# Performance work log

Measured on AMD Instinct MI355X. Metric: run time of the kernel, lower is better.

The kernel has to match this reference:

```python
import jax, jax.numpy as jnp
import numpy as np

BZ, T, D, DFF, E, BEAMS = 128, 32, 768, 3072, 8, 2


def setup_inputs() -> dict:
    key = jax.random.key(0)
    ks = jax.random.split(key, 4)
    s = 0.02
    return {
        "x": jax.random.normal(ks[0], (BZ, T, D), jnp.float32),
        "attention_mask": jnp.ones((BZ, T), jnp.float32),
        "Wg": jax.random.normal(ks[1], (D, E), jnp.float32) * s,   # gate Linear(D,E,bias=False)
        "W1": jax.random.normal(ks[2], (E, D, DFF), jnp.float32) * s,
        "b1": jnp.zeros((E, DFF), jnp.float32),
        "W2": jax.random.normal(ks[3], (E, DFF, D), jnp.float32) * s,
        "b2": jnp.zeros((E, D), jnp.float32),
    }


def reference(x, attention_mask, Wg, W1, b1, W2, b2):
    # forward_gate: module builds its own all-ones mask regardless of input mask
    mask = jnp.ones((x.shape[0], x.shape[1]), x.dtype)
    x_avg = (x * mask[..., None]).sum(1) / mask[..., None].sum(1)   # [bz, D]
    prob = jax.nn.softmax(x_avg @ Wg, axis=-1)                       # [bz, E]
    # beam_search (layer_judge='first', pre-route): topk on exp(log(softmax)) == softmax probs
    scores = jnp.exp(jnp.log(prob))
    topv, topi = jax.lax.top_k(scores, BEAMS)                        # [bz, beams]
    beam_scores = topv.reshape(-1)                                   # [bz*beams]
    expert_route = topi.reshape(-1, 1)                                # [bz*beams, 1]
    sel = expert_route[:, -1]
    # replicate x per beam: [bz*beams, T, D]
    x_rep = jnp.broadcast_to(x[:, None], (x.shape[0], BEAMS, x.shape[1], x.shape[2]))
    x_rep = x_rep.reshape(-1, x.shape[1], x.shape[2])
    # per-sample expert FFN dispatch (dense masked loop over the E=8 experts)
    out = jnp.zeros_like(x_rep)
    for e in range(E):
        h = jax.nn.gelu(jnp.einsum('nsd,df->nsf', x_rep, W1[e]) + b1[e], approximate=False)
        ye = jnp.einsum('nsf,fd->nsd', h, W2[e]) + b2[e]
        out = jnp.where((sel == e)[:, None, None], ye, out)
    return (out, beam_scores, expert_route)
```

## Files before the change

kernel.cpp:

```cpp
#include <hip/hip_runtime.h>
#include <cstddef>
#include <cstdint>

#define BZd   128
#define Td    32
#define Dd    768
#define DFFd  3072
#define Ed    8
#define NBEAM 256
#define ROWS_TOT 8192
#define OUT_ELEMS 6291456
#define MAXTILES 72

typedef unsigned short u16;
typedef __attribute__((ext_vector_type(4))) unsigned short ushort4v;
typedef __attribute__((ext_vector_type(8))) short frag_ab;
typedef __attribute__((ext_vector_type(4))) float floatx4;

__device__ __forceinline__ u16 f2bf(float f) {
  unsigned int u = __builtin_bit_cast(unsigned int, f);
  u += 0x7FFFu + ((u >> 16) & 1u);
  return (u16)(u >> 16);
}

__device__ __forceinline__ void async_copy16(u16* lds, const u16* g) {
  __builtin_amdgcn_global_load_lds(
      (const __attribute__((address_space(1))) void*)g,
      (__attribute__((address_space(3))) void*)lds, 16, 0, 0);
}

__device__ __forceinline__ float gelu_fast(float x) {
  float z = 1.5957691216f * (x + 0.044715f * x * x * x);
  return x / (1.0f + __expf(-z));
}

__global__ __launch_bounds__(256) void route_convert_kernel(
    const float* __restrict__ x, const float* __restrict__ Wg,
    float* __restrict__ out, int* __restrict__ sel, u16* __restrict__ xbf) {
  int b = blockIdx.x;
  int t = threadIdx.x;
  __shared__ float red[256][8];
  float la[8];
#pragma unroll
  for (int e = 0; e < 8; e++) la[e] = 0.f;
  for (int d = t; d < Dd; d += 256) {
    const float* xp = x + (size_t)b * Td * Dd + d;
    float xa = 0.f;
#pragma unroll
    for (int tt = 0; tt < Td; tt++) xa += xp[(size_t)tt * Dd];
    xa *= (1.0f / 32.0f);
#pragma unroll
    for (int e = 0; e < 8; e++) la[e] += xa * Wg[d * 8 + e];
  }
#pragma unroll
  for (int e = 0; e < 8; e++) red[t][e] = la[e];
  __syncthreads();
  for (int s = 128; s > 0; s >>= 1) {
    if (t < s) {
#pragma unroll
      for (int e = 0; e < 8; e++) red[t][e] += red[t + s][e];
    }
    __syncthreads();
  }
  if (t == 0) {
    float lg[8];
#pragma unroll
    for (int e = 0; e < 8; e++) lg[e] = red[0][e];
    float mx = lg[0];
#pragma unroll
    for (int e = 1; e < 8; e++) mx = fmaxf(mx, lg[e]);
    float p[8];
    float sum = 0.f;
#pragma unroll
    for (int e = 0; e < 8; e++) { p[e] = __expf(lg[e] - mx); sum += p[e]; }
    float inv = 1.0f / sum;
#pragma unroll
    for (int e = 0; e < 8; e++) p[e] *= inv;
    int i0 = 0; float v0 = p[0];
#pragma unroll
    for (int e = 1; e < 8; e++) if (p[e] > v0) { v0 = p[e]; i0 = e; }
    int i1 = -1; float v1 = -1.0f;
#pragma unroll
    for (int e = 0; e < 8; e++) if (e != i0 && p[e] > v1) { v1 = p[e]; i1 = e; }
    float* bs = out + OUT_ELEMS;
    float* er = out + OUT_ELEMS + NBEAM;
    bs[2 * b] = v0; bs[2 * b + 1] = v1;
    er[2 * b] = (float)i0; er[2 * b + 1] = (float)i1;
    sel[2 * b] = i0; sel[2 * b + 1] = i1;
  }
  const float* xp = x + (size_t)b * Td * Dd;
  u16* op = xbf + (size_t)b * Td * Dd;
#pragma unroll
  for (int k = 0; k < 24; k++) {
    int flat = (k * 256 + t) * 4;
    float4 v = *(const float4*)(xp + flat);
    ushort4v pv = {f2bf(v.x), f2bf(v.y), f2bf(v.z), f2bf(v.w)};
    *(ushort4v*)(op + flat) = pv;
  }
}

__global__ __launch_bounds__(256) void bucket_kernel(
    const int* __restrict__ sel, int* __restrict__ perm, int4* __restrict__ tiles) {
  __shared__ int ssel[NBEAM];
  __shared__ int scnt[8];
  __shared__ int soff[8];
  __shared__ int sperm[NBEAM];
  int t = threadIdx.x;
  ssel[t] = sel[t];
  __syncthreads();
  if (t == 0) {
    for (int e = 0; e < 8; e++) scnt[e] = 0;
    for (int n = 0; n < NBEAM; n++) scnt[ssel[n]]++;
    int o = 0;
    for (int e = 0; e < 8; e++) { soff[e] = o; o += scnt[e]; }
  }
  __syncthreads();
  if (t < 8) {
    int idx = soff[t];
    for (int n = 0; n < NBEAM; n++)
      if (ssel[n] == t) sperm[idx++] = n;
  }
  if (t == 0) {
    int tt = 0;
    for (int e = 0; e < 8; e++) {
      int nr = scnt[e] * 32;
      int base = soff[e] * 32;
      for (int r0 = 0; r0 < nr; r0 += 128) {
        tiles[tt] = make_int4(e, base + r0, min(128, nr - r0), 0);
        tt++;
      }
    }
    for (; tt < MAXTILES; tt++) tiles[tt] = make_int4(-1, 0, 0, 0);
  }
  __syncthreads();
  perm[t] = sperm[t];
}

__global__ __launch_bounds__(256) void transpose_all_kernel(
    const float* __restrict__ W1, u16* __restrict__ w1t,
    const float* __restrict__ W2, u16* __restrict__ w2t, int f0, int FC) {
  __shared__ u16 tile[64][65];
  int z = blockIdx.z, bx = blockIdx.x, by = blockIdx.y;
  int t = threadIdx.x;
  const float* ip; u16* op; int ld_in, ld_out;
  if (z < 8) {
    int e = z;
    ld_in = DFFd; ld_out = Dd;
    ip = W1 + (size_t)e * Dd * DFFd + (size_t)(bx * 64) * DFFd + (f0 + by * 64);
    op = w1t + (size_t)e * FC * Dd + (size_t)(by * 64) * Dd + bx * 64;
  } else {
    int e = z - 8;
    ld_in = Dd; ld_out = FC;
    ip = W2 + (size_t)e * DFFd * Dd + (size_t)(f0 + by * 64) * Dd + bx * 64;
    op = w2t + (size_t)e * Dd * FC + (size_t)(bx * 64) * FC + by * 64;
  }
  int rr = t >> 4, cc4 = (t & 15) * 4;
#pragma unroll
  for (int i = 0; i < 4; i++) {
    int r = rr + 16 * i;
    float4 v = *(const float4*)(ip + (size_t)r * ld_in + cc4);
    tile[r][cc4 + 0] = f2bf(v.x);
    tile[r][cc4 + 1] = f2bf(v.y);
    tile[r][cc4 + 2] = f2bf(v.z);
    tile[r][cc4 + 3] = f2bf(v.w);
  }
  __syncthreads();
  int ccw = t >> 4, r4 = (t & 15) * 4;
#pragma unroll
  for (int i = 0; i < 4; i++) {
    int cc = ccw + 16 * i;
    ushort4v pv = {tile[r4 + 0][cc], tile[r4 + 1][cc], tile[r4 + 2][cc], tile[r4 + 3][cc]};
    *(ushort4v*)(op + (size_t)cc * ld_out + r4) = pv;
  }
}

__global__ __launch_bounds__(256) void gemm1_kernel(
    const u16* __restrict__ xbf, const u16* __restrict__ w1t,
    const float* __restrict__ b1, const int* __restrict__ perm,
    const int4* __restrict__ tiles, u16* __restrict__ h, int f0, int FC) {
  int4 meta = tiles[blockIdx.y];
  int e = meta.x;
  if (e < 0) return;
  int grow0 = meta.y, nrows = meta.z;
  int bx = blockIdx.x;

  __shared__ __align__(16) u16 As[2][128 * 32];
  __shared__ __align__(16) u16 Bs[2][128 * 32];

  int t = threadIdx.x;
  int l = t & 63, w = t >> 6;
  int wm = w & 1, wn = w >> 1;
  int lrow = l & 15, lquad = l >> 4;

  const u16* ag[2]; const u16* bg[2];
  int lbase[2];
#pragma unroll
  for (int j = 0; j < 2; j++) {
    int s = j * 256 + t;
    int m = s >> 2;
    int koff = ((s & 3) ^ ((m >> 1) & 3)) * 8;
    int bidx = (grow0 >> 5) + (m >> 5);
    bidx = bidx < NBEAM ? bidx : NBEAM - 1;
    int batch = perm[bidx] >> 1;
    ag[j] = xbf + ((size_t)batch * Td + (m & 31)) * Dd + koff;
    bg[j] = w1t + ((size_t)e * FC + bx * 128 + m) * Dd + koff;
    lbase[j] = (j * 256 + w * 64) * 8;
  }

  int aoff[4], boff[4];
#pragma unroll
  for (int i = 0; i < 4; i++) {
    int ra = wm * 64 + i * 16 + lrow;
    aoff[i] = ra * 32 + ((lquad ^ ((ra >> 1) & 3)) * 8);
    int rb = wn * 64 + i * 16 + lrow;
    boff[i] = rb * 32 + ((lquad ^ ((rb >> 1) & 3)) * 8);
  }

  floatx4 acc[4][4];
#pragma unroll
  for (int mi = 0; mi < 4; mi++)
#pragma unroll
    for (int ni = 0; ni < 4; ni++) acc[mi][ni] = (floatx4){0.f, 0.f, 0.f, 0.f};

#pragma unroll
  for (int j = 0; j < 2; j++) {
    async_copy16(&As[0][lbase[j]], ag[j]);
    async_copy16(&Bs[0][lbase[j]], bg[j]);
    ag[j] += 32; bg[j] += 32;
  }

  const int NIT = Dd / 32;
  for (int it = 0; it < NIT; ++it) {
    __syncthreads();
    int cur = it & 1, nxt = cur ^ 1;
    if (it + 1 < NIT) {
#pragma unroll
      for (int j = 0; j < 2; j++) {
        async_copy16(&As[nxt][lbase[j]], ag[j]);
        async_copy16(&Bs[nxt][lbase[j]], bg[j]);
        ag[j] += 32; bg[j] += 32;
      }
    }
    frag_ab af[4], bf[4];
#pragma unroll
    for (int mi = 0; mi < 4; mi++) af[mi] = *(const frag_ab*)(&As[cur][aoff[mi]]);
#pragma unroll
    for (int ni = 0; ni < 4; ni++) bf[ni] = *(const frag_ab*)(&Bs[cur][boff[ni]]);
#pragma unroll
    for (int mi = 0; mi < 4; mi++)
#pragma unroll
      for (int ni = 0; ni < 4; ni++)
        acc[mi][ni] = __builtin_amdgcn_mfma_f32_16x16x32_bf16(af[mi], bf[ni], acc[mi][ni], 0, 0, 0);
  }

  int f_base = bx * 128;
#pragma unroll
  for (int mi = 0; mi < 4; mi++) {
    int row0 = wm * 64 + mi * 16 + lquad * 4;
#pragma unroll
    for (int ni = 0; ni < 4; ni++) {
      int col = wn * 64 + ni * 16 + lrow;
      float bias = b1[(size_t)e * DFFd + f0 + f_base + col];
#pragma unroll
      for (int r = 0; r < 4; r++) {
        int row = row0 + r;
        if (row < nrows) {
          float vv = acc[mi][ni][r] + bias;
          h[(size_t)(grow0 + row) * FC + f_base + col] = f2bf(gelu_fast(vv));
        }
      }
    }
  }
}

__global__ __launch_bounds__(256) void gemm2_kernel(
    const u16* __restrict__ h, const u16* __restrict__ w2t,
    const float* __restrict__ b2, const int* __restrict__ perm,
    const int4* __restrict__ tiles, float* __restrict__ out,
    int FC, int first) {
  int4 meta = tiles[blockIdx.y];
  int e = meta.x;
  if (e < 0) return;
  int grow0 = meta.y, nrows = meta.z;
  int bx = blockIdx.x;

  __shared__ __align__(16) u16 As[2][128 * 32];
  __shared__ __align__(16) u16 Bs[2][128 * 32];
  __shared__ int sbeam[4];

  int t = threadIdx.x;
  if (t < 4) {
    int idx = (grow0 >> 5) + t;
    sbeam[t] = perm[idx < NBEAM ? idx : NBEAM - 1];
  }
  int l = t & 63, w = t >> 6;
  int wm = w & 1, wn = w >> 1;
  int lrow = l & 15, lquad = l >> 4;

  const u16* ag[2]; const u16* bg[2];
  int lbase[2];
#pragma unroll
  for (int j = 0; j < 2; j++) {
    int s = j * 256 + t;
    int m = s >> 2;
    int koff = ((s & 3) ^ ((m >> 1) & 3)) * 8;
    int arow = grow0 + m;
    arow = arow < ROWS_TOT ? arow : ROWS_TOT - 1;
    ag[j] = h + (size_t)arow * FC + koff;
    bg[j] = w2t + ((size_t)e * Dd + bx * 128 + m) * FC + koff;
    lbase[j] = (j * 256 + w * 64) * 8;
  }

  int aoff[4], boff[4];
#pragma unroll
  for (int i = 0; i < 4; i++) {
    int ra = wm * 64 + i * 16 + lrow;
    aoff[i] = ra * 32 + ((lquad ^ ((ra >> 1) & 3)) * 8);
    int rb = wn * 64 + i * 16 + lrow;
    boff[i] = rb * 32 + ((lquad ^ ((rb >> 1) & 3)) * 8);
  }

  floatx4 acc[4][4];
#pragma unroll
  for (int mi = 0; mi < 4; mi++)
#pragma unroll
    for (int ni = 0; ni < 4; ni++) acc[mi][ni] = (floatx4){0.f, 0.f, 0.f, 0.f};

#pragma unroll
  for (int j = 0; j < 2; j++) {
    async_copy16(&As[0][lbase[j]], ag[j]);
    async_copy16(&Bs[0][lbase[j]], bg[j]);
    ag[j] += 32; bg[j] += 32;
  }

  const int NIT_ = FC / 32;
  for (int it = 0; it < NIT_; ++it) {
    __syncthreads();
    int cur = it & 1, nxt = cur ^ 1;
    if (it + 1 < NIT_) {
#pragma unroll
      for (int j = 0; j < 2; j++) {
        async_copy16(&As[nxt][lbase[j]], ag[j]);
        async_copy16(&Bs[nxt][lbase[j]], bg[j]);
        ag[j] += 32; bg[j] += 32;
      }
    }
    frag_ab af[4], bf[4];
#pragma unroll
    for (int mi = 0; mi < 4; mi++) af[mi] = *(const frag_ab*)(&As[cur][aoff[mi]]);
#pragma unroll
    for (int ni = 0; ni < 4; ni++) bf[ni] = *(const frag_ab*)(&Bs[cur][boff[ni]]);
#pragma unroll
    for (int mi = 0; mi < 4; mi++)
#pragma unroll
      for (int ni = 0; ni < 4; ni++)
        acc[mi][ni] = __builtin_amdgcn_mfma_f32_16x16x32_bf16(af[mi], bf[ni], acc[mi][ni], 0, 0, 0);
  }

#pragma unroll
  for (int mi = 0; mi < 4; mi++) {
    int row0 = wm * 64 + mi * 16 + lquad * 4;
#pragma unroll
    for (int ni = 0; ni < 4; ni++) {
      int col = wn * 64 + ni * 16 + lrow;
      int dg = bx * 128 + col;
      float bias = b2[(size_t)e * Dd + dg];
#pragma unroll
      for (int r = 0; r < 4; r++) {
        int row = row0 + r;
        if (row < nrows) {
          int beam = sbeam[row >> 5];
          size_t o = ((size_t)beam * Td + (row & 31)) * Dd + dg;
          if (first) out[o] = acc[mi][ni][r] + bias;
          else out[o] += acc[mi][ni][r];
        }
      }
    }
  }
}

extern "C" void kernel_launch(void* const* d_in, const int* in_sizes, int n_in,
                              void* d_out, int out_size, void* d_ws, size_t ws_size,
                              hipStream_t stream) {
  const float* x  = (const float*)d_in[0];
  const float* Wg = (const float*)d_in[2];
  const float* W1 = (const float*)d_in[3];
  const float* b1 = (const float*)d_in[4];
  const float* W2 = (const float*)d_in[5];
  const float* b2 = (const float*)d_in[6];
  float* out = (float*)d_out;

  char* ws = (char*)d_ws;
  int*  sel   = (int*)ws;
  int*  perm  = sel + NBEAM;
  int4* tiles = (int4*)(ws + 4096);

  const size_t xbf_off = 65536;
  const size_t xbf_bytes = (size_t)BZd * Td * Dd * 2;
  int FC = 384;
  if      (xbf_off + xbf_bytes + (size_t)40960 * 3072 <= ws_size) FC = 3072;
  else if (xbf_off + xbf_bytes + (size_t)40960 * 1536 <= ws_size) FC = 1536;
  else if (xbf_off + xbf_bytes + (size_t)40960 * 768  <= ws_size) FC = 768;
  int NC = DFFd / FC;

  u16* xbf = (u16*)(ws + xbf_off);
  u16* w1t = (u16*)(ws + xbf_off + xbf_bytes);
  u16* w2t = w1t + (size_t)Ed * FC * Dd;
  u16* h   = w2t + (size_t)Ed * Dd * FC;

  route_convert_kernel<<<BZd, 256, 0, stream>>>(x, Wg, out, sel, xbf);
  bucket_kernel<<<1, 256, 0, stream>>>(sel, perm, tiles);

  for (int c = 0; c < NC; c++) {
    transpose_all_kernel<<<dim3(Dd / 64, FC / 64, 16), 256, 0, stream>>>(
        W1, w1t, W2, w2t, c * FC, FC);
    gemm1_kernel<<<dim3(FC / 128, MAXTILES), 256, 0, stream>>>(
        xbf, w1t, b1, perm, tiles, h, c * FC, FC);
    gemm2_kernel<<<dim3(Dd / 128, MAXTILES), 256, 0, stream>>>(
        h, w2t, b2, perm, tiles, out, FC, c == 0 ? 1 : 0);
  }
}
```

Before: 401.2 us.

## Enlarge GEMM tiles and K-steps, drop double buffering in expert FFN kernels

gemm1 now computes 128x256 tiles with each wave owning a full-M 128x64 slice, and uses a K step of 64. gemm2 uses a K step of 128. Both kernels switch from double-buffered async copies to a single buffer that is loaded, synced, computed and synced again. The minimum feature chunk FC rises to 768. The aim is fewer barriers per FLOP and more reuse per LDS load. The cost is losing load/compute overlap, needing more LDS and registers (gemm1 uses 32 accumulators per lane), and launching fewer gemm1 blocks.

Result: slower. 451.3 us (+12.5%).

```diff
diff --git a/kernel.cpp b/kernel.cpp
--- a/kernel.cpp
+++ b/kernel.cpp
@@ -184,82 +184,87 @@
   int grow0 = meta.y, nrows = meta.z;
   int bx = blockIdx.x;
 
-  __shared__ __align__(16) u16 As[2][128 * 32];
-  __shared__ __align__(16) u16 Bs[2][128 * 32];
+  __shared__ __align__(16) u16 As[128 * 64];
+  __shared__ __align__(16) u16 Bs[256 * 64];
 
   int t = threadIdx.x;
   int l = t & 63, w = t >> 6;
-  int wm = w & 1, wn = w >> 1;
   int lrow = l & 15, lquad = l >> 4;
 
-  const u16* ag[2]; const u16* bg[2];
-  int lbase[2];
-#pragma unroll
-  for (int j = 0; j < 2; j++) {
+  const u16* ag[4];
+  int albase[4];
+#pragma unroll
+  for (int j = 0; j < 4; j++) {
     int s = j * 256 + t;
-    int m = s >> 2;
-    int koff = ((s & 3) ^ ((m >> 1) & 3)) * 8;
+    int m = s >> 3;
+    int koff = ((s & 7) ^ ((m >> 1) & 7)) * 8;
     int bidx = (grow0 >> 5) + (m >> 5);
     bidx = bidx < NBEAM ? bidx : NBEAM - 1;
     int batch = perm[bidx] >> 1;
     ag[j] = xbf + ((size_t)batch * Td + (m & 31)) * Dd + koff;
-    bg[j] = w1t + ((size_t)e * FC + bx * 128 + m) * Dd + koff;
-    lbase[j] = (j * 256 + w * 64) * 8;
-  }
-
-  int aoff[4], boff[4];
-#pragma unroll
-  for (int i = 0; i < 4; i++) {
-    int ra = wm * 64 + i * 16 + lrow;
-    aoff[i] = ra * 32 + ((lquad ^ ((ra >> 1) & 3)) * 8);
-    int rb = wn * 64 + i * 16 + lrow;
-    boff[i] = rb * 32 + ((lquad ^ ((rb >> 1) & 3)) * 8);
-  }
-
-  floatx4 acc[4][4];
-#pragma unroll
-  for (int mi = 0; mi < 4; mi++)
+    albase[j] = (j * 256 + w * 64) * 8;
+  }
+  const u16* bg[8];
+  int blbase[8];
+#pragma unroll
+  for (int j = 0; j < 8; j++) {
+    int s = j * 256 + t;
+    int m = s >> 3;
+    int koff = ((s & 7) ^ ((m >> 1) & 7)) * 8;
+    bg[j] = w1t + ((size_t)e * FC + bx * 256 + m) * Dd + koff;
+    blbase[j] = (j * 256 + w * 64) * 8;
+  }
+
+  int aoff[2][8], boff[2][4];
+#pragma unroll
+  for (int hh = 0; hh < 2; hh++) {
+#pragma unroll
+    for (int mi = 0; mi < 8; mi++) {
+      int ra = mi * 16 + lrow;
+      aoff[hh][mi] = ra * 64 + (((lquad + hh * 4) ^ ((ra >> 1) & 7)) * 8);
+    }
+#pragma unroll
+    for (int ni = 0; ni < 4; ni++) {
+      int rb = w * 64 + ni * 16 + lrow;
+      boff[hh][ni] = rb * 64 + (((lquad + hh * 4) ^ ((rb >> 1) & 7)) * 8);
+    }
+  }
+
+  floatx4 acc[8][4];
+#pragma unroll
+  for (int mi = 0; mi < 8; mi++)
 #pragma unroll
     for (int ni = 0; ni < 4; ni++) acc[mi][ni] = (floatx4){0.f, 0.f, 0.f, 0.f};
 
-#pragma unroll
-  for (int j = 0; j < 2; j++) {
-    async_copy16(&As[0][lbase[j]], ag[j]);
-    async_copy16(&Bs[0][lbase[j]], bg[j]);
-    ag[j] += 32; bg[j] += 32;
-  }
-
-  const int NIT = Dd / 32;
-  for (int it = 0; it < NIT; ++it) {
+  for (int kt = 0; kt < Dd; kt += 64) {
+#pragma unroll
+    for (int j = 0; j < 4; j++) { async_copy16(&As[albase[j]], ag[j]); ag[j] += 64; }
+#pragma unroll
+    for (int j = 0; j < 8; j++) { async_copy16(&Bs[blbase[j]], bg[j]); bg[j] += 64; }
     __syncthreads();
-    int cur = it & 1, nxt = cur ^ 1;
-    if (it + 1 < NIT) {
-#pragma unroll
-      for (int j = 0; j < 2; j++) {
-        async_copy16(&As[nxt][lbase[j]], ag[j]);
-        async_copy16(&Bs[nxt][lbase[j]], bg[j]);
-        ag[j] += 32; bg[j] += 32;
-      }
-    }
-    frag_ab af[4], bf[4];
-#pragma unroll
-    for (int mi = 0; mi < 4; mi++) af[mi] = *(const frag_ab*)(&As[cur][aoff[mi]]);
-#pragma unroll
-    for (int ni = 0; ni < 4; ni++) bf[ni] = *(const frag_ab*)(&Bs[cur][boff[ni]]);
-#pragma unroll
-    for (int mi = 0; mi < 4; mi++)
-#pragma unroll
-      for (int ni = 0; ni < 4; ni++)
-        acc[mi][ni] = __builtin_amdgcn_mfma_f32_16x16x32_bf16(af[mi], bf[ni], acc[mi][ni], 0, 0, 0);
-  }
-
-  int f_base = bx * 128;
-#pragma unroll
-  for (int mi = 0; mi < 4; mi++) {
-    int row0 = wm * 64 + mi * 16 + lquad * 4;
+#pragma unroll
+    for (int hh = 0; hh < 2; hh++) {
+      frag_ab af[8], bf[4];
+#pragma unroll
+      for (int mi = 0; mi < 8; mi++) af[mi] = *(const frag_ab*)(&As[aoff[hh][mi]]);
+#pragma unroll
+      for (int ni = 0; ni < 4; ni++) bf[ni] = *(const frag_ab*)(&Bs[boff[hh][ni]]);
+#pragma unroll
+      for (int mi = 0; mi < 8; mi++)
+#pragma unroll
+        for (int ni = 0; ni < 4; ni++)
+          acc[mi][ni] = __builtin_amdgcn_mfma_f32_16x16x32_bf16(af[mi], bf[ni], acc[mi][ni], 0, 0, 0);
+    }
+    __syncthreads();
+  }
+
+  int f_base = bx * 256;
+#pragma unroll
+  for (int mi = 0; mi < 8; mi++) {
+    int row0 = mi * 16 + lquad * 4;
 #pragma unroll
     for (int ni = 0; ni < 4; ni++) {
-      int col = wn * 64 + ni * 16 + lrow;
+      int col = w * 64 + ni * 16 + lrow;
       float bias = b1[(size_t)e * DFFd + f0 + f_base + col];
 #pragma unroll
       for (int r = 0; r < 4; r++) {
@@ -284,8 +289,8 @@
   int grow0 = meta.y, nrows = meta.z;
   int bx = blockIdx.x;
 
-  __shared__ __align__(16) u16 As[2][128 * 32];
-  __shared__ __align__(16) u16 Bs[2][128 * 32];
+  __shared__ __align__(16) u16 As[128 * 128];
+  __shared__ __align__(16) u16 Bs[128 * 128];
   __shared__ int sbeam[4];
 
   int t = threadIdx.x;
@@ -297,13 +302,13 @@
   int wm = w & 1, wn = w >> 1;
   int lrow = l & 15, lquad = l >> 4;
 
-  const u16* ag[2]; const u16* bg[2];
-  int lbase[2];
-#pragma unroll
-  for (int j = 0; j < 2; j++) {
+  const u16* ag[8]; const u16* bg[8];
+  int lbase[8];
+#pragma unroll
+  for (int j = 0; j < 8; j++) {
     int s = j * 256 + t;
-    int m = s >> 2;
-    int koff = ((s & 3) ^ ((m >> 1) & 3)) * 8;
+    int m = s >> 4;
+    int koff = ((s & 15) ^ ((m >> 1) & 7)) * 8;
     int arow = grow0 + m;
     arow = arow < ROWS_TOT ? arow : ROWS_TOT - 1;
     ag[j] = h + (size_t)arow * FC + koff;
@@ -311,14 +316,16 @@
     lbase[j] = (j * 256 + w * 64) * 8;
   }
 
-  int aoff[4], boff[4];
-#pragma unroll
-  for (int i = 0; i < 4; i++) {
-    int ra = wm * 64 + i * 16 + lrow;
-    aoff[i] = ra * 32 + ((lquad ^ ((ra >> 1) & 3)) * 8);
-    int rb = wn * 64 + i * 16 + lrow;
-    boff[i] = rb * 32 + ((lquad ^ ((rb >> 1) & 3)) * 8);
-  }
+  int aoff[4][4], boff[4][4];
+#pragma unroll
+  for (int hh = 0; hh < 4; hh++)
+#pragma unroll
+    for (int i = 0; i < 4; i++) {
+      int ra = wm * 64 + i * 16 + lrow;
+      aoff[hh][i] = ra * 128 + (((lquad + hh * 4) ^ ((ra >> 1) & 7)) * 8);
+      int rb = wn * 64 + i * 16 + lrow;
+      boff[hh][i] = rb * 128 + (((lquad + hh * 4) ^ ((rb >> 1) & 7)) * 8);
+    }
 
   floatx4 acc[4][4];
 #pragma unroll
@@ -326,35 +333,28 @@
 #pragma unroll
     for (int ni = 0; ni < 4; ni++) acc[mi][ni] = (floatx4){0.f, 0.f, 0.f, 0.f};
 
-#pragma unroll
-  for (int j = 0; j < 2; j++) {
-    async_copy16(&As[0][lbase[j]], ag[j]);
-    async_copy16(&Bs[0][lbase[j]], bg[j]);
-    ag[j] += 32; bg[j] += 32;
-  }
-
-  const int NIT_ = FC / 32;
-  for (int it = 0; it < NIT_; ++it) {
+  for (int kt = 0; kt < FC; kt += 128) {
+#pragma unroll
+    for (int j = 0; j < 8; j++) {
+      async_copy16(&As[lbase[j]], ag[j]);
+      async_copy16(&Bs[lbase[j]], bg[j]);
+      ag[j] += 128; bg[j] += 128;
+    }
     __syncthreads();
-    int cur = it & 1, nxt = cur ^ 1;
-    if (it + 1 < NIT_) {
-#pragma unroll
-      for (int j = 0; j < 2; j++) {
-        async_copy16(&As[nxt][lbase[j]], ag[j]);
-        async_copy16(&Bs[nxt][lbase[j]], bg[j]);
-        ag[j] += 32; bg[j] += 32;
-      }
-    }
-    frag_ab af[4], bf[4];
-#pragma unroll
-    for (int mi = 0; mi < 4; mi++) af[mi] = *(const frag_ab*)(&As[cur][aoff[mi]]);
-#pragma unroll
-    for (int ni = 0; ni < 4; ni++) bf[ni] = *(const frag_ab*)(&Bs[cur][boff[ni]]);
-#pragma unroll
-    for (int mi = 0; mi < 4; mi++)
-#pragma unroll
-      for (int ni = 0; ni < 4; ni++)
-        acc[mi][ni] = __builtin_amdgcn_mfma_f32_16x16x32_bf16(af[mi], bf[ni], acc[mi][ni], 0, 0, 0);
+#pragma unroll
+    for (int hh = 0; hh < 4; hh++) {
+      frag_ab af[4], bf[4];
+#pragma unroll
+      for (int mi = 0; mi < 4; mi++) af[mi] = *(const frag_ab*)(&As[aoff[hh][mi]]);
+#pragma unroll
+      for (int ni = 0; ni < 4; ni++) bf[ni] = *(const frag_ab*)(&Bs[boff[hh][ni]]);
+#pragma unroll
+      for (int mi = 0; mi < 4; mi++)
+#pragma unroll
+        for (int ni = 0; ni < 4; ni++)
+          acc[mi][ni] = __builtin_amdgcn_mfma_f32_16x16x32_bf16(af[mi], bf[ni], acc[mi][ni], 0, 0, 0);
+    }
+    __syncthreads();
   }
 
 #pragma unroll
@@ -397,10 +397,9 @@
 
   const size_t xbf_off = 65536;
   const size_t xbf_bytes = (size_t)BZd * Td * Dd * 2;
-  int FC = 384;
+  int FC = 768;
   if      (xbf_off + xbf_bytes + (size_t)40960 * 3072 <= ws_size) FC = 3072;
   else if (xbf_off + xbf_bytes + (size_t)40960 * 1536 <= ws_size) FC = 1536;
-  else if (xbf_off + xbf_bytes + (size_t)40960 * 768  <= ws_size) FC = 768;
   int NC = DFFd / FC;
 
   u16* xbf = (u16*)(ws + xbf_off);
@@ -414,7 +413,7 @@
   for (int c = 0; c < NC; c++) {
     transpose_all_kernel<<<dim3(Dd / 64, FC / 64, 16), 256, 0, stream>>>(
         W1, w1t, W2, w2t, c * FC, FC);
-    gemm1_kernel<<<dim3(FC / 128, MAXTILES), 256, 0, stream>>>(
+    gemm1_kernel<<<dim3(FC / 256, MAXTILES), 256, 0, stream>>>(
         xbf, w1t, b1, perm, tiles, h, c * FC, FC);
     gemm2_kernel<<<dim3(Dd / 128, MAXTILES), 256, 0, stream>>>(
         h, w2t, b2, perm, tiles, out, FC, c == 0 ? 1 : 0);
```
